# Performance work log

Hardware: AMD Instinct MI355X
Metric: run time of the kernel (lower is better)

The kernel has to match this reference:

```python
import jax, jax.numpy as jnp
import numpy as np

B, TAU, D, DX, DZ, H = 512, 4, 5, 256, 16, 64
M = D * DZ
COEFF_KL = 1.0
LOG2PI = float(np.log(2.0 * np.pi))


def setup_inputs() -> dict:
    ks = jax.random.split(jax.random.key(0), 12)
    s = 0.05
    return {
        "x": jax.random.normal(ks[0], (B, TAU, D, DX), jnp.float32),
        "y": jax.random.normal(ks[1], (B, D, DX), jnp.float32),
        "mask_param": jnp.full((TAU, M, M), 5.0, jnp.float32),
        "w_enc": ((0.9 * jax.random.uniform(ks[2], (D, DZ, DX)) + 0.1) / DX).astype(jnp.float32),
        "w_dec": ((0.9 * jax.random.uniform(ks[3], (D, DX, DZ)) + 0.1) / DZ).astype(jnp.float32),
        "enc_W0": jax.random.normal(ks[4], (DZ, DX, H), jnp.float32) * s,
        "enc_b0": jnp.zeros((DZ, H), jnp.float32),
        "enc_W1": jax.random.normal(ks[5], (DZ, H), jnp.float32) * s,
        "enc_b1": jnp.zeros((DZ,), jnp.float32),
        "dec_W0": jax.random.normal(ks[6], (DX, DZ, H), jnp.float32) * s,
        "dec_b0": jnp.zeros((DX, H), jnp.float32),
        "dec_W1": jax.random.normal(ks[7], (DX, H), jnp.float32) * s,
        "dec_b1": jnp.zeros((DX,), jnp.float32),
        "t_W0": jax.random.normal(ks[8], (M, TAU * M, H), jnp.float32) * s,
        "t_b0": jnp.zeros((M, H), jnp.float32),
        "t_W1": jax.random.normal(ks[9], (M, H), jnp.float32) * s,
        "t_b1": jnp.zeros((M,), jnp.float32),
        "logvar_enc": jnp.full((D,), -1.0, jnp.float32),
        "logvar_dec": jnp.full((D,), -1.0, jnp.float32),
        "t_logvar": jnp.full((D, DZ), -4.0, jnp.float32),
    }


def _encode(x, w_enc, W0, b0, W1, b1):
    # x: (..., D, DX) -> mu: (..., D, DZ); d_z tiny MLPs gated by mixing weights
    masked = w_enc * x[..., None, :]  # (..., D, DZ, DX)
    h = jax.nn.leaky_relu(jnp.einsum('...ijx,jxh->...ijh', masked, W0) + b0)
    return jnp.einsum('...ijh,jh->...ij', h, W1) + b1


def _forward(x, y, mask_param, w_enc, w_dec, enc_W0, enc_b0, enc_W1, enc_b1,
             dec_W0, dec_b0, dec_W1, dec_b1, t_W0, t_b0, t_W1, t_b1,
             logvar_enc, logvar_dec, t_logvar):
    b = x.shape[0]
    k_adj, k_ep, k_et = jax.random.split(jax.random.key(42), 3)
    # gumbel-sigmoid soft adjacency sample (temperature 1, drawhard=False)
    u = jax.random.uniform(k_adj, (b, TAU, M, M), minval=1e-6, maxval=1.0 - 1e-6)
    adj = jax.nn.sigmoid(mask_param + jnp.log(u) - jnp.log1p(-u))  # (b,TAU,M,M)
    # encoder q(z|x): reparameterized gaussian, per-feature logvar
    q_std = jnp.exp(0.5 * logvar_enc)[:, None]                     # (D,1)
    mu_past = _encode(x, w_enc, enc_W0, enc_b0, enc_W1, enc_b1)    # (b,TAU,D,DZ)
    z_past = mu_past + q_std * jax.random.normal(k_ep, mu_past.shape, jnp.float32)
    mu_t = _encode(y, w_enc, enc_W0, enc_b0, enc_W1, enc_b1)       # (b,D,DZ)
    z_t = mu_t + q_std * jax.random.normal(k_et, mu_t.shape, jnp.float32)
    # transition p(z_t|z_<t): per-node MLP on adjacency-gated past latents
    zp = z_past.reshape(b, TAU, M)
    gated = adj * zp[:, :, None, :]                                # (b,TAU,node,src)
    gated = gated.transpose(0, 2, 1, 3).reshape(b, M, TAU * M)
    ht = jax.nn.leaky_relu(jnp.einsum('bmi,mih->bmh', gated, t_W0) + t_b0)
    pz_mu = (jnp.einsum('bmh,mh->bm', ht, t_W1) + t_b1).reshape(b, D, DZ)
    pz_std = jnp.exp(0.5 * t_logvar)                               # (D,DZ)
    # decoder p(x|z): d_x tiny MLPs on mixing-mask-gated latents
    masked_z = w_dec * z_t[:, :, None, :]                          # (b,D,DX,DZ)
    hd = jax.nn.leaky_relu(jnp.einsum('bijz,jzh->bijh', masked_z, dec_W0) + dec_b0)
    px_mu = jnp.einsum('bijh,jh->bij', hd, dec_W1) + dec_b1        # (b,D,DX)
    px_std = jnp.exp(0.5 * logvar_dec)[:, None]                    # (D,1)
    # ELBO: gaussian recon log-lik + analytic gaussian KL(q || p_transition)
    recon = -0.5 * ((y - px_mu) / px_std) ** 2 - jnp.log(px_std) - 0.5 * LOG2PI
    recon = recon.sum(axis=(1, 2)).mean()
    kl = (jnp.log(pz_std) - 0.5 * logvar_enc[:, None]
          + (q_std ** 2 + (mu_t - pz_mu) ** 2) / (2.0 * pz_std ** 2) - 0.5)
    kl = kl.sum(axis=(1, 2)).mean()
    return -(recon - COEFF_KL * kl)


def reference(x, y, mask_param, w_enc, w_dec, enc_W0, enc_b0, enc_W1, enc_b1,
              dec_W0, dec_b0, dec_W1, dec_b1, t_W0, t_b0, t_W1, t_b1,
              logvar_enc, logvar_dec, t_logvar):
    return _forward(x, y, mask_param, w_enc, w_dec, enc_W0, enc_b0, enc_W1, enc_b1,
                    dec_W0, dec_b0, dec_W1, dec_b1, t_W0, t_b0, t_W1, t_b1,
                    logvar_enc, logvar_dec, t_logvar)
```

## Files before the change

kernel.cpp:

```cpp
#include <hip/hip_runtime.h>
#include <cstdint>

constexpr int NB = 512, NTAU = 4, ND = 5, NDX = 256, NDZ = 16, NH = 64;
constexpr int NM  = ND * NDZ;
constexpr int NTM = NTAU * NM;
constexpr int NSAMP = NB * NTAU + NB;
constexpr float LOG2PI_F = 1.8378770664093453f;

typedef __attribute__((ext_vector_type(8))) short bf16x8;
typedef __attribute__((ext_vector_type(4))) float f32x4;

__device__ __forceinline__ unsigned long long mix64(unsigned long long z) {
  z += 0x9E3779B97F4A7C15ull;
  z = (z ^ (z >> 30)) * 0xBF58476D1CE4E5B9ull;
  z = (z ^ (z >> 27)) * 0x94D049BB133111EBull;
  return z ^ (z >> 31);
}
__device__ __forceinline__ float u01f(unsigned long long h) {
  return ((float)(unsigned)(h >> 40) + 0.5f) * (1.0f / 16777216.0f);
}
__device__ __forceinline__ float rng_normal(unsigned long long salt, unsigned long long idx) {
  float u1 = u01f(mix64(salt + 2ull * idx));
  float u2 = u01f(mix64(salt + 2ull * idx + 1ull));
  float r = sqrtf(-2.0f * logf(u1));
  return r * cosf(6.283185307179586f * u2);
}
constexpr unsigned long long SALT_ADJ = 0x1000000000000ull;
constexpr unsigned long long SALT_EP  = 0x2000000000000ull;
constexpr unsigned long long SALT_ET  = 0x3000000000000ull;

__device__ __forceinline__ short f2bf(float f) {
  unsigned u = __float_as_uint(f);
  unsigned r = (u + 0x7FFFu + ((u >> 16) & 1u)) >> 16;
  return (short)r;
}

__global__ __launch_bounds__(256) void k_prepP(
    const float* __restrict__ w_enc, const float* __restrict__ eW0,
    short* __restrict__ PtE)
{
  __shared__ float lds[64][65];
  const int bid = blockIdx.x;
  const int d  = bid >> 6;
  const int z  = (bid & 63) >> 2;
  const int k0 = (bid & 3) * 64;
  const int tid = threadIdx.x;

  for (int i = tid; i < 64 * 64; i += 256) {
    int kk = i >> 6, h = i & 63;
    lds[kk][h] = eW0[((size_t)z * NDX + k0 + kk) * NH + h];
  }
  __syncthreads();
  for (int i = tid; i < 64 * 64; i += 256) {
    int h = i >> 6, kk = i & 63;
    float v = w_enc[((size_t)d * NDZ + z) * NDX + k0 + kk] * lds[kk][h];
    PtE[((size_t)(d * 1024 + z * 64 + h)) * NDX + k0 + kk] = f2bf(v);
  }
}

__global__ __launch_bounds__(512) void k_enc_mfma(
    const float* __restrict__ x, const float* __restrict__ y,
    const short* __restrict__ PtE,
    const float* __restrict__ b0, const float* __restrict__ W1,
    const float* __restrict__ b1, const float* __restrict__ lve,
    float* __restrict__ z_past, float* __restrict__ mu_t, float* __restrict__ z_t,
    const float* __restrict__ w_dec, const float* __restrict__ dW0,
    short* __restrict__ QtD,
    const float* __restrict__ tW0, short* __restrict__ TtB,
    float* __restrict__ yT)
{
  __shared__ __align__(16) char smem[35840];
  const int bid = blockIdx.x;
  const int tid = threadIdx.x;

  if (bid < 400) {
    short* Bs = (short*)smem;
    float (*mu_s)[4] = (float(*)[4])(smem + 33792);

    const int d = bid / 80;
    const int r80 = bid % 80;
    const int zq = r80 / 20;
    const int s0 = (r80 % 20) * 128;
    const int w = tid >> 6, l = tid & 63;
    const int lrow = l & 15, g = l >> 4;

    const int srow = s0 + w * 16 + lrow;
    const float* Asrc = (srow < NB * NTAU)
        ? &x[((size_t)srow * ND + d) * NDX]
        : &y[((size_t)(srow - NB * NTAU) * ND + d) * NDX];
    bf16x8 a[8];
    #pragma unroll
    for (int ks = 0; ks < 8; ++ks) {
      const float* p = Asrc + g * 8 + ks * 32;
      float4 f0 = *(const float4*)p;
      float4 f1 = *(const float4*)(p + 4);
      a[ks][0] = f2bf(f0.x); a[ks][1] = f2bf(f0.y);
      a[ks][2] = f2bf(f0.z); a[ks][3] = f2bf(f0.w);
      a[ks][4] = f2bf(f1.x); a[ks][5] = f2bf(f1.y);
      a[ks][6] = f2bf(f1.z); a[ks][7] = f2bf(f1.w);
    }

    const int stg_row = tid >> 3;
    const int stg_c   = (tid & 7) * 32;

    for (int zi = 0; zi < 4; ++zi) {
      const int z = zq * 4 + zi;
      {
        const short* src = PtE + ((size_t)(d * 1024 + z * 64 + stg_row)) * NDX + stg_c;
        short* dst = Bs + stg_row * 264 + stg_c;
        #pragma unroll
        for (int j = 0; j < 4; ++j)
          *(bf16x8*)(dst + j * 8) = *(const bf16x8*)(src + j * 8);
      }
      __syncthreads();

      f32x4 acc[4] = {};
      #pragma unroll
      for (int nt = 0; nt < 4; ++nt) {
        const short* Brow = Bs + (nt * 16 + lrow) * 264 + g * 8;
        #pragma unroll
        for (int ks = 0; ks < 8; ++ks) {
          bf16x8 bv = *(const bf16x8*)(Brow + ks * 32);
          acc[nt] = __builtin_amdgcn_mfma_f32_16x16x32_bf16(a[ks], bv, acc[nt], 0, 0, 0);
        }
      }

      float b0v[4], w1v[4];
      #pragma unroll
      for (int nt = 0; nt < 4; ++nt) {
        int h = nt * 16 + lrow;
        b0v[nt] = b0[z * NH + h];
        w1v[nt] = W1[z * NH + h];
      }
      const float b1v = b1[z];
      #pragma unroll
      for (int reg = 0; reg < 4; ++reg) {
        float v = 0.0f;
        #pragma unroll
        for (int nt = 0; nt < 4; ++nt) {
          float hv = acc[nt][reg] + b0v[nt];
          hv = fmaxf(hv, 0.01f * hv);
          v += hv * w1v[nt];
        }
        #pragma unroll
        for (int off = 1; off < 16; off <<= 1) v += __shfl_xor(v, off, 16);
        if (lrow == 0)
          mu_s[w * 16 + g * 4 + reg][zi] = v + b1v;
      }
      __syncthreads();
    }

    {
      const int sl = tid >> 2, zi = tid & 3;
      const int z = zq * 4 + zi;
      const int s = s0 + sl;
      const int m = d * NDZ + z;
      float mu = mu_s[sl][zi];
      float qs = expf(0.5f * lve[d]);
      if (s < NB * NTAU) {
        float eps = rng_normal(SALT_EP, (unsigned long long)s * NM + m);
        z_past[(size_t)s * NM + m] = mu + qs * eps;
      } else {
        int b = s - NB * NTAU;
        float eps = rng_normal(SALT_ET, (unsigned long long)b * NM + m);
        size_t o = (size_t)b * NM + m;
        mu_t[o] = mu;
        z_t[o]  = mu + qs * eps;
      }
    }
  } else if (bid < 560) {
    int t = (bid - 400) * 512 + tid;
    int d = t / (NDX * NH);
    int r = t % (NDX * NH);
    int xx = r >> 6, h = r & 63;
    size_t base = (size_t)t * 32;
    #pragma unroll
    for (int z = 0; z < NDZ; ++z)
      QtD[base + z] = f2bf(w_dec[((size_t)d * NDX + xx) * NDZ + z] *
                           dW0[((size_t)xx * NDZ + z) * NH + h]);
    #pragma unroll
    for (int z = NDZ; z < 32; ++z) QtD[base + z] = 0;
  } else if (bid < 960) {
    short (*lds)[65] = (short(*)[65])smem;
    int r = bid - 560;
    int kt = r % 5, m = r / 5;
    int k0 = kt * 64;
    for (int idx = tid; idx < 64 * 64; idx += 512) {
      int hh = idx & 63, kk = idx >> 6;
      lds[kk][hh] = f2bf(tW0[((size_t)m * NTM + k0 + kk) * NH + hh]);
    }
    __syncthreads();
    for (int idx = tid; idx < 64 * 64; idx += 512) {
      int kk = idx & 63, hh = idx >> 6;
      TtB[((size_t)m * NH + hh) * NTM + k0 + kk] = lds[kk][hh];
    }
  } else {
    int e0 = ((bid - 960) * 512 + tid) * 4;
    int d = e0 / (NDX * NB);
    int rem = e0 % (NDX * NB);
    int xx = rem >> 9, b0i = rem & 511;
    float4 o;
    o.x = y[((size_t)(b0i + 0) * ND + d) * NDX + xx];
    o.y = y[((size_t)(b0i + 1) * ND + d) * NDX + xx];
    o.z = y[((size_t)(b0i + 2) * ND + d) * NDX + xx];
    o.w = y[((size_t)(b0i + 3) * ND + d) * NDX + xx];
    *(float4*)&yT[e0] = o;
  }
}

__global__ __launch_bounds__(512) void k_tail(
    const float* __restrict__ mask_param, const float* __restrict__ z_past,
    const short* __restrict__ TtB,
    const float* __restrict__ tb0, const float* __restrict__ tW1,
    const float* __restrict__ tb1, const float* __restrict__ lve,
    const float* __restrict__ t_logvar, const float* __restrict__ mu_t,
    float* __restrict__ kl_partial,
    const float* __restrict__ zt, const short* __restrict__ QtD,
    const float* __restrict__ yT, const float* __restrict__ db0,
    const float* __restrict__ dW1, const float* __restrict__ db1,
    const float* __restrict__ lvd, float* __restrict__ rec_partial)
{
  __shared__ float ems[NTM];
  __shared__ float redb[8];

  const int bid = blockIdx.x;
  const int tid = threadIdx.x;

  if (bid < 320) {
    const int m = bid >> 2;
    const int b0 = (bid & 3) * 128;
    const int w = tid >> 6, l = tid & 63;
    const int lrow = l & 15, g = l >> 4;

    for (int i = tid; i < NTM; i += 512) {
      int t = i / NM, s = i - t * NM;
      ems[i] = expf(-mask_param[(t * NM + m) * NM + s]);
    }
    __syncthreads();

    const int brow = b0 + w * 16 + lrow;
    const float* zrow = z_past + (size_t)brow * NTM;
    bf16x8 a[10];
    #pragma unroll
    for (int ks = 0; ks < 10; ++ks) {
      const int tm0 = g * 8 + ks * 32;
      const int t = tm0 / NM;
      const int s0 = tm0 - t * NM;
      unsigned long long aibase =
          ((unsigned long long)((brow * NTAU + t) * NM + m)) * NM + s0;
      unsigned long long h0 = mix64(SALT_ADJ + aibase);
      unsigned long long h1 = mix64(SALT_ADJ + aibase + 2);
      unsigned long long h2 = mix64(SALT_ADJ + aibase + 4);
      unsigned long long h3 = mix64(SALT_ADJ + aibase + 6);
      float u[8];
      u[0] = ((float)(unsigned)(h0 >> 40) + 0.5f) * (1.0f / 16777216.0f);
      u[1] = ((float)((unsigned)(h0 >> 16) & 0xFFFFFFu) + 0.5f) * (1.0f / 16777216.0f);
      u[2] = ((float)(unsigned)(h1 >> 40) + 0.5f) * (1.0f / 16777216.0f);
      u[3] = ((float)((unsigned)(h1 >> 16) & 0xFFFFFFu) + 0.5f) * (1.0f / 16777216.0f);
      u[4] = ((float)(unsigned)(h2 >> 40) + 0.5f) * (1.0f / 16777216.0f);
      u[5] = ((float)((unsigned)(h2 >> 16) & 0xFFFFFFu) + 0.5f) * (1.0f / 16777216.0f);
      u[6] = ((float)(unsigned)(h3 >> 40) + 0.5f) * (1.0f / 16777216.0f);
      u[7] = ((float)((unsigned)(h3 >> 16) & 0xFFFFFFu) + 0.5f) * (1.0f / 16777216.0f);
      float4 z0 = *(const float4*)(zrow + tm0);
      float4 z1 = *(const float4*)(zrow + tm0 + 4);
      const float* zvp0 = &z0.x;
      const float* zvp1 = &z1.x;
      #pragma unroll
      for (int j = 0; j < 8; ++j) {
        float uu = fminf(fmaxf(u[j], 1e-6f), 1.0f - 1e-6f);
        float e = ems[tm0 + j];
        float den = fmaf(e, 1.0f - uu, uu);
        float adj = uu * __builtin_amdgcn_rcpf(den);
        float zv = (j < 4) ? zvp0[j] : zvp1[j - 4];
        a[ks][j] = f2bf(adj * zv);
      }
    }

    f32x4 acc[4] = {};
    #pragma unroll
    for (int nt = 0; nt < 4; ++nt) {
      const short* Brow = TtB + ((size_t)(m * NH + nt * 16 + lrow)) * NTM + g * 8;
      #pragma unroll
      for (int ks = 0; ks < 10; ++ks) {
        bf16x8 bv = *(const bf16x8*)(Brow + ks * 32);
        acc[nt] = __builtin_amdgcn_mfma_f32_16x16x32_bf16(a[ks], bv, acc[nt], 0, 0, 0);
      }
    }

    float b0v[4], w1v[4];
    #pragma unroll
    for (int nt = 0; nt < 4; ++nt) {
      int h = nt * 16 + lrow;
      b0v[nt] = tb0[m * NH + h];
      w1v[nt] = tW1[m * NH + h];
    }

    const int d = m >> 4;
    const float lv_t = t_logvar[m];
    const float lv_e = lve[d];
    const float inv2var = 0.5f * expf(-lv_t);
    const float qvar = expf(lv_e);
    const float cterm = 0.5f * lv_t - 0.5f * lv_e - 0.5f;
    const float bv1 = tb1[m];

    float klw = 0.0f;
    #pragma unroll
    for (int reg = 0; reg < 4; ++reg) {
      float v = 0.0f;
      #pragma unroll
      for (int nt = 0; nt < 4; ++nt) {
        float hv = acc[nt][reg] + b0v[nt];
        hv = fmaxf(hv, 0.01f * hv);
        v += hv * w1v[nt];
      }
      #pragma unroll
      for (int off = 1; off < 16; off <<= 1) v += __shfl_xor(v, off, 16);
      if (lrow == 0) {
        int b = b0 + w * 16 + g * 4 + reg;
        float pz = v + bv1;
        float diff = mu_t[(size_t)b * NM + m] - pz;
        klw += cterm + (qvar + diff * diff) * inv2var;
      }
    }
    klw += __shfl_xor(klw, 16, 64);
    klw += __shfl_xor(klw, 32, 64);

    if (l == 0) redb[w] = klw;
    __syncthreads();
    if (tid == 0) {
      float s = 0.f;
      #pragma unroll
      for (int i = 0; i < 8; ++i) s += redb[i];
      kl_partial[(bid & 3) * NM + m] = s;
    }
  } else {
    const int idx = bid - 320;
    const int d = idx >> 8, xx = idx & 255;
    const int w8 = tid >> 6, l = tid & 63;
    const int mb = w8 >> 2, w = w8 & 3;
    const int lrow = l & 15, g = l >> 4;

    bf16x8 bfr[4];
    const short* Bbase = QtD + ((size_t)((d * NDX + xx) * NH)) * 32;
    #pragma unroll
    for (int nt = 0; nt < 4; ++nt)
      bfr[nt] = *(const bf16x8*)(Bbase + (nt * 16 + lrow) * 32 + g * 8);

    f32x4 acc[4][4] = {};
    #pragma unroll
    for (int mt = 0; mt < 4; ++mt) {
      int b = mb * 256 + w * 64 + mt * 16 + lrow;
      bf16x8 a = {0, 0, 0, 0, 0, 0, 0, 0};
      if (g < 2) {
        const float* zp = zt + (size_t)b * NM + d * NDZ + g * 8;
        float4 f0 = *(const float4*)zp;
        float4 f1 = *(const float4*)(zp + 4);
        a[0] = f2bf(f0.x); a[1] = f2bf(f0.y); a[2] = f2bf(f0.z); a[3] = f2bf(f0.w);
        a[4] = f2bf(f1.x); a[5] = f2bf(f1.y); a[6] = f2bf(f1.z); a[7] = f2bf(f1.w);
      }
      #pragma unroll
      for (int nt = 0; nt < 4; ++nt)
        acc[mt][nt] = __builtin_amdgcn_mfma_f32_16x16x32_bf16(a, bfr[nt], acc[mt][nt], 0, 0, 0);
    }

    float db0v[4], dW1v[4];
    #pragma unroll
    for (int nt = 0; nt < 4; ++nt) {
      int h = nt * 16 + lrow;
      db0v[nt] = db0[xx * NH + h];
      dW1v[nt] = dW1[xx * NH + h];
    }
    const float lv = lvd[d];
    const float inv_std = expf(-0.5f * lv);
    const float cterm = -0.5f * lv - 0.5f * LOG2PI_F;
    const float b1v = db1[xx];

    float racc = 0.0f;
    #pragma unroll
    for (int mt = 0; mt < 4; ++mt) {
      float rs[4];
      #pragma unroll
      for (int reg = 0; reg < 4; ++reg) {
        float v = 0.0f;
        #pragma unroll
        for (int nt = 0; nt < 4; ++nt) {
          float hv = acc[mt][nt][reg] + db0v[nt];
          hv = fmaxf(hv, 0.01f * hv);
          v += hv * dW1v[nt];
        }
        #pragma unroll
        for (int off = 1; off < 16; off <<= 1) v += __shfl_xor(v, off, 16);
        rs[reg] = v;
      }
      if (lrow == 0) {
        int b = mb * 256 + w * 64 + mt * 16 + g * 4;
        float4 yv = *(const float4*)&yT[((size_t)d * NDX + xx) * NB + b];
        const float* yvp = &yv.x;
        #pragma unroll
        for (int reg = 0; reg < 4; ++reg) {
          float px = rs[reg] + b1v;
          float e = (yvp[reg] - px) * inv_std;
          racc += -0.5f * e * e + cterm;
        }
      }
    }
    racc += __shfl_xor(racc, 16, 64);
    racc += __shfl_xor(racc, 32, 64);

    if (l == 0) redb[w8] = racc;
    __syncthreads();
    if (tid == 0) {
      float s = 0.f;
      #pragma unroll
      for (int i = 0; i < 8; ++i) s += redb[i];
      rec_partial[(size_t)d * NDX + xx] = s;
    }
  }
}

__global__ __launch_bounds__(256) void k_reduce(
    const float* __restrict__ rp, const float* __restrict__ kp,
    float* __restrict__ out)
{
  __shared__ float sr[4], sk[4];
  float r = 0.f, k = 0.f;
  for (int i = threadIdx.x; i < 1280; i += 256) r += rp[i];
  for (int i = threadIdx.x; i < 320; i += 256) k += kp[i];
  #pragma unroll
  for (int off = 32; off; off >>= 1) {
    r += __shfl_xor(r, off, 64);
    k += __shfl_xor(k, off, 64);
  }
  int wv = threadIdx.x >> 6;
  if ((threadIdx.x & 63) == 0) { sr[wv] = r; sk[wv] = k; }
  __syncthreads();
  if (threadIdx.x == 0) {
    float R = sr[0] + sr[1] + sr[2] + sr[3];
    float K = sk[0] + sk[1] + sk[2] + sk[3];
    out[0] = (K - R) / (float)NB;
  }
}

extern "C" void kernel_launch(void* const* d_in, const int* in_sizes, int n_in,
                              void* d_out, int out_size, void* d_ws, size_t ws_size,
                              hipStream_t stream) {
  (void)in_sizes; (void)n_in; (void)out_size; (void)ws_size;
  const float* x        = (const float*)d_in[0];
  const float* y        = (const float*)d_in[1];
  const float* mask_p   = (const float*)d_in[2];
  const float* w_enc    = (const float*)d_in[3];
  const float* w_dec    = (const float*)d_in[4];
  const float* enc_W0   = (const float*)d_in[5];
  const float* enc_b0   = (const float*)d_in[6];
  const float* enc_W1   = (const float*)d_in[7];
  const float* enc_b1   = (const float*)d_in[8];
  const float* dec_W0   = (const float*)d_in[9];
  const float* dec_b0   = (const float*)d_in[10];
  const float* dec_W1   = (const float*)d_in[11];
  const float* dec_b1   = (const float*)d_in[12];
  const float* t_W0     = (const float*)d_in[13];
  const float* t_b0     = (const float*)d_in[14];
  const float* t_W1     = (const float*)d_in[15];
  const float* t_b1     = (const float*)d_in[16];
  const float* lv_enc   = (const float*)d_in[17];
  const float* lv_dec   = (const float*)d_in[18];
  const float* t_logvar = (const float*)d_in[19];

  float* ws     = (float*)d_ws;
  float* z_past = ws;
  float* mu_t   = z_past + 163840;
  float* z_t    = mu_t + 40960;
  float* rec_p  = z_t + 40960;
  float* kl_p   = rec_p + 1280;
  float* yTb    = kl_p + 320;
  short* PtE    = (short*)(yTb + 655360);
  short* QtD    = PtE + 5 * 1024 * NDX;
  short* TtB    = QtD + 5 * NDX * NH * 32;

  k_prepP<<<320, 256, 0, stream>>>(w_enc, enc_W0, PtE);
  k_enc_mfma<<<1280, 512, 0, stream>>>(
      x, y, PtE, enc_b0, enc_W1, enc_b1, lv_enc,
      z_past, mu_t, z_t, w_dec, dec_W0, QtD, t_W0, TtB, yTb);
  k_tail<<<1600, 512, 0, stream>>>(
      mask_p, z_past, TtB, t_b0, t_W1, t_b1, lv_enc, t_logvar, mu_t, kl_p,
      z_t, QtD, yTb, dec_b0, dec_W1, dec_b1, lv_dec, rec_p);
  k_reduce<<<1, 256, 0, stream>>>(rec_p, kl_p, (float*)d_out);
}
```

Measured before the change: 72.62 us.

## Split transition K-loop across wave halves with LDS reduction in k_tail

The transition-MLP part of k_tail now uses twice as many blocks, each covering 64 batch rows instead of 128. The 8 waves in a block split the K dimension into two halves, and partial MFMA accumulators are combined through a shared-memory buffer. The goal is more parallelism and shorter per-wave serial latency from RNG generation and MFMA chains. In exchange it adds 16 KB of LDS per block, an extra barrier, and more KL partials for the final reduce.

Result: slower. 77.16 us (+6.3%).

```diff
diff --git a/kernel.cpp b/kernel.cpp
--- a/kernel.cpp
+++ b/kernel.cpp
@@ -221,15 +221,17 @@
     const float* __restrict__ lvd, float* __restrict__ rec_partial)
 {
   __shared__ float ems[NTM];
+  __shared__ float accs[16][4][64];
   __shared__ float redb[8];
 
   const int bid = blockIdx.x;
   const int tid = threadIdx.x;
 
-  if (bid < 320) {
-    const int m = bid >> 2;
-    const int b0 = (bid & 3) * 128;
+  if (bid < 640) {
+    const int m = bid >> 3;
+    const int b0 = (bid & 7) * 64;
     const int w = tid >> 6, l = tid & 63;
+    const int bsub = w & 3, kh = w >> 2;
     const int lrow = l & 15, g = l >> 4;
 
     for (int i = tid; i < NTM; i += 512) {
@@ -238,11 +240,13 @@
     }
     __syncthreads();
 
-    const int brow = b0 + w * 16 + lrow;
+    const int brow = b0 + bsub * 16 + lrow;
     const float* zrow = z_past + (size_t)brow * NTM;
-    bf16x8 a[10];
-    #pragma unroll
-    for (int ks = 0; ks < 10; ++ks) {
+
+    f32x4 acc[4] = {};
+    #pragma unroll
+    for (int kk = 0; kk < 5; ++kk) {
+      const int ks = kh * 5 + kk;
       const int tm0 = g * 8 + ks * 32;
       const int t = tm0 / NM;
       const int s0 = tm0 - t * NM;
@@ -265,6 +269,7 @@
       float4 z1 = *(const float4*)(zrow + tm0 + 4);
       const float* zvp0 = &z0.x;
       const float* zvp1 = &z1.x;
+      bf16x8 a;
       #pragma unroll
       for (int j = 0; j < 8; ++j) {
         float uu = fminf(fmaxf(u[j], 1e-6f), 1.0f - 1e-6f);
@@ -272,69 +277,72 @@
         float den = fmaf(e, 1.0f - uu, uu);
         float adj = uu * __builtin_amdgcn_rcpf(den);
         float zv = (j < 4) ? zvp0[j] : zvp1[j - 4];
-        a[ks][j] = f2bf(adj * zv);
-      }
-    }
-
-    f32x4 acc[4] = {};
-    #pragma unroll
-    for (int nt = 0; nt < 4; ++nt) {
-      const short* Brow = TtB + ((size_t)(m * NH + nt * 16 + lrow)) * NTM + g * 8;
-      #pragma unroll
-      for (int ks = 0; ks < 10; ++ks) {
+        a[j] = f2bf(adj * zv);
+      }
+      #pragma unroll
+      for (int nt = 0; nt < 4; ++nt) {
+        const short* Brow = TtB + ((size_t)(m * NH + nt * 16 + lrow)) * NTM + g * 8;
         bf16x8 bv = *(const bf16x8*)(Brow + ks * 32);
-        acc[nt] = __builtin_amdgcn_mfma_f32_16x16x32_bf16(a[ks], bv, acc[nt], 0, 0, 0);
-      }
-    }
-
-    float b0v[4], w1v[4];
-    #pragma unroll
-    for (int nt = 0; nt < 4; ++nt) {
-      int h = nt * 16 + lrow;
-      b0v[nt] = tb0[m * NH + h];
-      w1v[nt] = tW1[m * NH + h];
-    }
-
-    const int d = m >> 4;
-    const float lv_t = t_logvar[m];
-    const float lv_e = lve[d];
-    const float inv2var = 0.5f * expf(-lv_t);
-    const float qvar = expf(lv_e);
-    const float cterm = 0.5f * lv_t - 0.5f * lv_e - 0.5f;
-    const float bv1 = tb1[m];
-
-    float klw = 0.0f;
-    #pragma unroll
-    for (int reg = 0; reg < 4; ++reg) {
-      float v = 0.0f;
+        acc[nt] = __builtin_amdgcn_mfma_f32_16x16x32_bf16(a, bv, acc[nt], 0, 0, 0);
+      }
+    }
+
+    if (kh == 1) {
+      #pragma unroll
+      for (int k = 0; k < 16; ++k)
+        accs[k][bsub][l] = acc[k >> 2][k & 3];
+    }
+    __syncthreads();
+
+    if (kh == 0) {
+      #pragma unroll
+      for (int k = 0; k < 16; ++k)
+        acc[k >> 2][k & 3] += accs[k][bsub][l];
+
+      float b0v[4], w1v[4];
       #pragma unroll
       for (int nt = 0; nt < 4; ++nt) {
-        float hv = acc[nt][reg] + b0v[nt];
-        hv = fmaxf(hv, 0.01f * hv);
-        v += hv * w1v[nt];
-      }
-      #pragma unroll
-      for (int off = 1; off < 16; off <<= 1) v += __shfl_xor(v, off, 16);
-      if (lrow == 0) {
-        int b = b0 + w * 16 + g * 4 + reg;
-        float pz = v + bv1;
-        float diff = mu_t[(size_t)b * NM + m] - pz;
-        klw += cterm + (qvar + diff * diff) * inv2var;
-      }
-    }
-    klw += __shfl_xor(klw, 16, 64);
-    klw += __shfl_xor(klw, 32, 64);
-
-    if (l == 0) redb[w] = klw;
+        int h = nt * 16 + lrow;
+        b0v[nt] = tb0[m * NH + h];
+        w1v[nt] = tW1[m * NH + h];
+      }
+
+      const int d = m >> 4;
+      const float lv_t = t_logvar[m];
+      const float lv_e = lve[d];
+      const float inv2var = 0.5f * expf(-lv_t);
+      const float qvar = expf(lv_e);
+      const float cterm = 0.5f * lv_t - 0.5f * lv_e - 0.5f;
+      const float bv1 = tb1[m];
+
+      float klw = 0.0f;
+      #pragma unroll
+      for (int reg = 0; reg < 4; ++reg) {
+        float v = 0.0f;
+        #pragma unroll
+        for (int nt = 0; nt < 4; ++nt) {
+          float hv = acc[nt][reg] + b0v[nt];
+          hv = fmaxf(hv, 0.01f * hv);
+          v += hv * w1v[nt];
+        }
+        #pragma unroll
+        for (int off = 1; off < 16; off <<= 1) v += __shfl_xor(v, off, 16);
+        if (lrow == 0) {
+          int b = b0 + bsub * 16 + g * 4 + reg;
+          float pz = v + bv1;
+          float diff = mu_t[(size_t)b * NM + m] - pz;
+          klw += cterm + (qvar + diff * diff) * inv2var;
+        }
+      }
+      klw += __shfl_xor(klw, 16, 64);
+      klw += __shfl_xor(klw, 32, 64);
+      if (l == 0) redb[bsub] = klw;
+    }
     __syncthreads();
-    if (tid == 0) {
-      float s = 0.f;
-      #pragma unroll
-      for (int i = 0; i < 8; ++i) s += redb[i];
-      kl_partial[(bid & 3) * NM + m] = s;
-    }
+    if (tid == 0)
+      kl_partial[bid] = redb[0] + redb[1] + redb[2] + redb[3];
   } else {
-    const int idx = bid - 320;
+    const int idx = bid - 640;
     const int d = idx >> 8, xx = idx & 255;
     const int w8 = tid >> 6, l = tid & 63;
     const int mb = w8 >> 2, w = w8 & 3;
@@ -425,7 +433,7 @@
   __shared__ float sr[4], sk[4];
   float r = 0.f, k = 0.f;
   for (int i = threadIdx.x; i < 1280; i += 256) r += rp[i];
-  for (int i = threadIdx.x; i < 320; i += 256) k += kp[i];
+  for (int i = threadIdx.x; i < 640; i += 256) k += kp[i];
   #pragma unroll
   for (int off = 32; off; off >>= 1) {
     r += __shfl_xor(r, off, 64);
@@ -472,7 +480,7 @@
   float* z_t    = mu_t + 40960;
   float* rec_p  = z_t + 40960;
   float* kl_p   = rec_p + 1280;
-  float* yTb    = kl_p + 320;
+  float* yTb    = kl_p + 640;
   short* PtE    = (short*)(yTb + 655360);
   short* QtD    = PtE + 5 * 1024 * NDX;
   short* TtB    = QtD + 5 * NDX * NH * 32;
@@ -481,7 +489,7 @@
   k_enc_mfma<<<1280, 512, 0, stream>>>(
       x, y, PtE, enc_b0, enc_W1, enc_b1, lv_enc,
       z_past, mu_t, z_t, w_dec, dec_W0, QtD, t_W0, TtB, yTb);
-  k_tail<<<1600, 512, 0, stream>>>(
+  k_tail<<<1920, 512, 0, stream>>>(
       mask_p, z_past, TtB, t_b0, t_W1, t_b1, lv_enc, t_logvar, mu_t, kl_p,
       z_t, QtD, yTb, dec_b0, dec_W1, dec_b1, lv_dec, rec_p);
   k_reduce<<<1, 256, 0, stream>>>(rec_p, kl_p, (float*)d_out);
```
